# Kernel optimization log

Hardware: AMD Instinct MI355X
Metric: run time of the kernel (lower is better)

## Reference

```python
import jax, jax.numpy as jnp
import numpy as np

B, S, H = 4, 2048, 1024
N_EXPERTS = 8
EXPERT_DIM = 1024  # must equal H (see module: wo features = expert_dim, output added to zeros_like(x))
TOP_K = 2
Z_LOSS_COEF = 0.001


def setup_inputs() -> dict:
    key = jax.random.key(0)
    ks = jax.random.split(key, 8)
    s_h = 1.0 / np.sqrt(H)
    s_e = 1.0 / np.sqrt(EXPERT_DIM)
    return {
        "x": jax.random.normal(ks[0], (B, S, H), dtype=jnp.float32),
        "router_w": jax.random.normal(ks[1], (H, N_EXPERTS), dtype=jnp.float32) * s_h,
        "router_b": jnp.zeros((N_EXPERTS,), dtype=jnp.float32),
        "wi_w": jax.random.normal(ks[2], (N_EXPERTS, H, EXPERT_DIM), dtype=jnp.float32) * s_h,
        "wi_b": jnp.zeros((N_EXPERTS, EXPERT_DIM), dtype=jnp.float32),
        "wo_w": jax.random.normal(ks[3], (N_EXPERTS, EXPERT_DIM, EXPERT_DIM), dtype=jnp.float32) * s_e,
        "wo_b": jnp.zeros((N_EXPERTS, EXPERT_DIM), dtype=jnp.float32),
    }


def reference(x, router_w, router_b, wi_w, wi_b, wo_w, wo_b):
    # Router (deterministic=True: no jitter noise, no dropout)
    logits = jnp.einsum("bsh,he->bse", x, router_w) + router_b        # [B,S,Ne]
    probs = jax.nn.softmax(logits, axis=-1)
    z_loss = jnp.mean(jnp.square(jax.nn.logsumexp(logits, axis=-1))) * Z_LOSS_COEF
    topk_p, topk_i = jax.lax.top_k(probs, TOP_K)                      # [B,S,2]
    topk_p = topk_p / jnp.sum(topk_p, axis=-1, keepdims=True)
    # Faithful to source: mask[...,None] ([B,S,2,1]) broadcasts against x ([B,S,H])
    # producing [B,S,2,H]; combined output has that shape.
    out = jnp.zeros((B, S, TOP_K, H), dtype=x.dtype)
    n_experts = wi_w.shape[0]
    for e in range(n_experts):  # fixed small expert loop, as in source
        mask = (topk_i == e)                                          # [B,S,2]
        p = jnp.where(mask, topk_p, 0.0)                              # [B,S,2]
        xin = jnp.where(mask[..., None], x[:, :, None, :], 0.0)       # [B,S,2,H]
        h = jax.nn.gelu(jnp.einsum("bskh,hd->bskd", xin, wi_w[e]) + wi_b[e])
        y = jnp.einsum("bskd,do->bsko", h, wo_w[e]) + wo_b[e]         # [B,S,2,H]
        out = out + y * p[..., None]
    return out, z_loss
```

## Files before the change

### kernel.cpp

```cpp
#include <hip/hip_runtime.h>

typedef unsigned short u16;
typedef unsigned int   u32;
typedef __bf16 bf16x8 __attribute__((ext_vector_type(8)));
typedef float  f32x4  __attribute__((ext_vector_type(4)));

#define NTOK   8192
#define NSLOT  16384

#define XB_OFF   0UL
#define WIT_OFF  16777216UL
#define WOT_OFF  33554432UL
#define HB_OFF   50331648UL
#define RE_OFF   83886080UL
#define RP_OFF   83951616UL
#define SEG_OFF  84017152UL
#define META_OFF 84082688UL
#define ZB_OFF   (META_OFF + 4096UL)
#define WS_NEED  (ZB_OFF + 32768UL)

__device__ __forceinline__ u16 f2b(float f) {
  u32 u = __float_as_uint(f);
  u32 r = (u + 0x7fffu + ((u >> 16) & 1u)) >> 16;
  return (u16)r;
}

__device__ __forceinline__ void async_cp16(const void* g, void* l) {
  __builtin_amdgcn_global_load_lds(
      (const __attribute__((address_space(1))) u32*)g,
      (__attribute__((address_space(3))) u32*)l, 16, 0, 0);
}

__device__ __forceinline__ float gelu_f(float v) {
  float u  = 0.7978845608028654f * (v + 0.044715f * v * v * v);
  float ex = __expf(2.0f * u);
  float th = 1.0f - 2.0f / (ex + 1.0f);
  return 0.5f * v * (1.0f + th);
}

__global__ __launch_bounds__(256) void k_transpose(const float* __restrict__ wi,
                                                   const float* __restrict__ wo,
                                                   u16* __restrict__ wit,
                                                   u16* __restrict__ wot) {
  __shared__ float t[64][65];
  int z = blockIdx.z;
  int e = z & 7;
  const float* src = ((z < 8) ? wi : wo) + ((size_t)e << 20);
  u16* dst = ((z < 8) ? wit : wot) + ((size_t)e << 20);
  int h0 = blockIdx.y * 64, d0 = blockIdx.x * 64;
  int tid = threadIdx.x;
#pragma unroll
  for (int j = 0; j < 4; j++) {
    int f = tid + 256 * j;
    int r = f >> 4, c4 = f & 15;
    float4 v = *(const float4*)&src[(size_t)(h0 + r) * 1024 + d0 + c4 * 4];
    t[r][c4 * 4 + 0] = v.x; t[r][c4 * 4 + 1] = v.y;
    t[r][c4 * 4 + 2] = v.z; t[r][c4 * 4 + 3] = v.w;
  }
  __syncthreads();
#pragma unroll
  for (int j = 0; j < 4; j++) {
    int f = tid + 256 * j;
    int d = f >> 4, c4 = f & 15;
    u32 p0 = (u32)f2b(t[c4 * 4 + 0][d]) | ((u32)f2b(t[c4 * 4 + 1][d]) << 16);
    u32 p1 = (u32)f2b(t[c4 * 4 + 2][d]) | ((u32)f2b(t[c4 * 4 + 3][d]) << 16);
    u32* dp = (u32*)&dst[(size_t)(d0 + d) * 1024 + h0 + c4 * 4];
    dp[0] = p0; dp[1] = p1;
  }
}

__global__ __launch_bounds__(256) void k_router(const float* __restrict__ x,
    const float* __restrict__ rw, const float* __restrict__ rb,
    u16* __restrict__ xb, int* __restrict__ route_e, float* __restrict__ route_p,
    float* __restrict__ zbuf) {
  int wv = blockIdx.x * 4 + (threadIdx.x >> 6);
  int l = threadIdx.x & 63;
#pragma unroll 1
  for (int t = 0; t < 4; t++) {
    int tok = wv * 4 + t;
    const float* xrow = x + (size_t)tok * 1024;
    u16* xbrow = xb + (size_t)tok * 1024;
    float a[8] = {0.f, 0.f, 0.f, 0.f, 0.f, 0.f, 0.f, 0.f};
#pragma unroll
    for (int j = 0; j < 16; j++) {
      int c = j * 64 + l;
      float xj = xrow[c];
      xbrow[c] = f2b(xj);
      float4 w0 = *(const float4*)&rw[c * 8];
      float4 w1 = *(const float4*)&rw[c * 8 + 4];
      a[0] += xj * w0.x; a[1] += xj * w0.y; a[2] += xj * w0.z; a[3] += xj * w0.w;
      a[4] += xj * w1.x; a[5] += xj * w1.y; a[6] += xj * w1.z; a[7] += xj * w1.w;
    }
#pragma unroll
    for (int e = 0; e < 8; e++)
#pragma unroll
      for (int off = 32; off; off >>= 1) a[e] += __shfl_xor(a[e], off, 64);
    if (l == 0) {
#pragma unroll
      for (int e = 0; e < 8; e++) a[e] += rb[e];
      int e0 = 0; float b0 = a[0];
#pragma unroll
      for (int k = 1; k < 8; k++) if (a[k] > b0) { b0 = a[k]; e0 = k; }
      int e1 = -1; float b1 = -3.4e38f;
#pragma unroll
      for (int k = 0; k < 8; k++) { if (k == e0) continue; if (a[k] > b1) { b1 = a[k]; e1 = k; } }
      float s = 0.f;
#pragma unroll
      for (int k = 0; k < 8; k++) s += __expf(a[k] - b0);
      float lse = b0 + __logf(s);
      float q1 = __expf(b1 - b0);
      route_e[tok * 2 + 0] = e0; route_e[tok * 2 + 1] = e1;
      route_p[tok * 2 + 0] = 1.0f / (1.0f + q1);
      route_p[tok * 2 + 1] = q1 / (1.0f + q1);
      zbuf[tok] = lse * lse;
    }
  }
}

__global__ __launch_bounds__(256) void k_scan(
    const int* __restrict__ route_e, int* __restrict__ offs,
    int* __restrict__ cursors, int* __restrict__ ntiles,
    int* __restrict__ tile_e, int* __restrict__ tile_r0,
    const float* __restrict__ zbuf, float* __restrict__ zout) {
  __shared__ int cnt[8];
  __shared__ float zs[4];
  int tid = threadIdx.x;
  if (tid < 8) cnt[tid] = 0;
  __syncthreads();
  for (int i = tid; i < NSLOT; i += 256) atomicAdd(&cnt[route_e[i]], 1);
  float z = 0.f;
  for (int i = tid; i < NTOK; i += 256) z += zbuf[i];
#pragma unroll
  for (int off = 32; off; off >>= 1) z += __shfl_xor(z, off, 64);
  if ((tid & 63) == 0) zs[tid >> 6] = z;
  __syncthreads();
  if (tid == 0) {
    *zout = (zs[0] + zs[1] + zs[2] + zs[3]) * (0.001f / 8192.0f);
    int o = 0, nt = 0;
    offs[0] = 0;
    for (int e = 0; e < 8; e++) {
      int c = cnt[e];
      cursors[e] = o;
      for (int r = 0; r < c; r += 320) { tile_e[nt] = e; tile_r0[nt] = o + r; nt++; }
      o += c;
      offs[e + 1] = o;
    }
    *ntiles = nt;
  }
}

__global__ __launch_bounds__(256) void k_scatter(const int* __restrict__ route_e,
                                                 int* __restrict__ cursors,
                                                 int* __restrict__ seg) {
  int i = blockIdx.x * 256 + threadIdx.x;
  int e = route_e[i];
  int lane = threadIdx.x & 63;
#pragma unroll
  for (int ex = 0; ex < 8; ex++) {
    unsigned long long mask = __ballot(e == ex);
    if (e == ex) {
      int cnt = __popcll(mask);
      int leader = __ffsll((long long)mask) - 1;
      int base = 0;
      if (lane == leader) base = atomicAdd(&cursors[ex], cnt);
      base = __shfl(base, leader, 64);
      int rank = __popcll(mask & ((1ull << lane) - 1ull));
      seg[base + rank] = i;
    }
  }
}


#define BAR()    asm volatile("s_barrier" ::: "memory")
#define WAITV0() asm volatile("s_waitcnt vmcnt(0)" ::: "memory")

#define STAGE_A(B, KT, J) async_cp16(asrc[J] + (KT) * 64, &As[B][(w * 40 + (J) * 8) * 64])
#define STAGE_B(B, KT, J) async_cp16(bsrc[J] + (KT) * 64, &Bs[B][(w * 32 + (J) * 8) * 64])

#define PHASE(CUR, Q)                                                              \
  do {                                                                             \
    bf16x8 af[2][2], bfr[2][4];                                                    \
    _Pragma("unroll")                                                              \
    for (int kk = 0; kk < 2; kk++) {                                               \
      int c = ((kk * 4 + rh) ^ (rl & 7)) * 8;                                      \
      _Pragma("unroll")                                                            \
      for (int d = 0; d < 2; d++)                                                  \
        af[kk][d] = *(const bf16x8*)&As[CUR][(wr * 160 + (2 * (Q) + d) * 16 + rl) * 64 + c]; \
      _Pragma("unroll")                                                            \
      for (int n = 0; n < 4; n++)                                                  \
        bfr[kk][n] = *(const bf16x8*)&Bs[CUR][(wc * 64 + n * 16 + rl) * 64 + c];   \
    }                                                                              \
    __builtin_amdgcn_s_setprio(1);                                                 \
    _Pragma("unroll")                                                              \
    for (int kk = 0; kk < 2; kk++)                                                 \
      _Pragma("unroll")                                                            \
      for (int d = 0; d < 2; d++)                                                  \
        _Pragma("unroll")                                                          \
        for (int n = 0; n < 4; n++)                                                \
          acc[2 * (Q) + d][n] = __builtin_amdgcn_mfma_f32_16x16x32_bf16(           \
              af[kk][d], bfr[kk][n], acc[2 * (Q) + d][n], 0, 0, 0);                \
    __builtin_amdgcn_s_setprio(0);                                                 \
  } while (0)

#define GEMM_BODY()                                                                \
  _Pragma("unroll")                                                                \
  for (int j = 0; j < 5; j++) STAGE_A(0, 0, j);                                    \
  _Pragma("unroll")                                                                \
  for (int j = 0; j < 4; j++) STAGE_B(0, 0, j);                                    \
  WAITV0(); BAR();                                                                 \
  _Pragma("unroll 2")                                                              \
  for (int g = 0; g < 16; g++) {                                                   \
    int cur = g & 1, nxt = cur ^ 1;                                                \
    bool pf = (g < 15);                                                            \
    if (pf) { STAGE_A(nxt, g + 1, 0); STAGE_A(nxt, g + 1, 1); STAGE_A(nxt, g + 1, 2); \
              STAGE_B(nxt, g + 1, 0); STAGE_B(nxt, g + 1, 1); }                    \
    PHASE(cur, 0); BAR();                                                          \
    if (pf) { STAGE_A(nxt, g + 1, 3); STAGE_A(nxt, g + 1, 4);                      \
              STAGE_B(nxt, g + 1, 2); STAGE_B(nxt, g + 1, 3); }                    \
    PHASE(cur, 1); BAR();                                                          \
    PHASE(cur, 2); BAR();                                                          \
    PHASE(cur, 3); BAR();                                                          \
    PHASE(cur, 4);                                                                 \
    WAITV0(); BAR();                                                               \
  }

__global__ __launch_bounds__(512, 2) void k_gemm_h(
    const u16* __restrict__ xb, const u16* __restrict__ wit, const float* __restrict__ wib,
    u16* __restrict__ hb, const int* __restrict__ seg, const int* __restrict__ offs,
    const int* __restrict__ tile_e, const int* __restrict__ tile_r0,
    const int* __restrict__ ntiles) {
  __shared__ u16 As[2][320 * 64];
  __shared__ u16 Bs[2][256 * 64];
  int bid = blockIdx.x;
  int swz = (bid & 7) * 30 + (bid >> 3);
  int mt = swz >> 2;
  if (mt >= *ntiles) return;
  int n0 = (swz & 3) << 8;
  int e = tile_e[mt], r0 = tile_r0[mt], end = offs[e + 1];
  int tid = threadIdx.x;
  int w = tid >> 6, l = tid & 63;
  int lr = l >> 3, lc = l & 7;
  int cs = lc ^ lr;
  const u16* asrc[5];
  const u16* bsrc[4];
#pragma unroll
  for (int j = 0; j < 5; j++) {
    int gr = r0 + w * 40 + j * 8 + lr;
    int idx = seg[(gr < end) ? gr : r0];
    asrc[j] = xb + (size_t)(idx >> 1) * 1024 + cs * 8;
  }
#pragma unroll
  for (int j = 0; j < 4; j++)
    bsrc[j] = wit + ((size_t)e << 20) + (size_t)(n0 + w * 32 + j * 8 + lr) * 1024 + cs * 8;
  f32x4 acc[10][4];
  f32x4 z4 = {0.f, 0.f, 0.f, 0.f};
#pragma unroll
  for (int m = 0; m < 10; m++)
#pragma unroll
    for (int n = 0; n < 4; n++) acc[m][n] = z4;
  int wr = w >> 2, wc = w & 3;
  int rl = l & 15, rh = l >> 4;
  GEMM_BODY()
#pragma unroll
  for (int n = 0; n < 4; n++) {
    int col = n0 + wc * 64 + n * 16 + rl;
    float bias = wib[e * 1024 + col];
#pragma unroll
    for (int m = 0; m < 10; m++) {
      int rbase = r0 + wr * 160 + m * 16 + rh * 4;
#pragma unroll
      for (int j = 0; j < 4; j++) {
        int gr = rbase + j;
        if (gr < end)
          hb[(size_t)gr * 1024 + col] = f2b(gelu_f(acc[m][n][j] + bias));
      }
    }
  }
}

__global__ __launch_bounds__(512, 2) void k_gemm_o(
    const u16* __restrict__ hb, const u16* __restrict__ wot, const float* __restrict__ wob,
    float* __restrict__ out, const int* __restrict__ seg, const int* __restrict__ offs,
    const int* __restrict__ tile_e, const int* __restrict__ tile_r0,
    const int* __restrict__ ntiles, const float* __restrict__ route_p) {
  __shared__ u16 As[2][320 * 64];
  __shared__ u16 Bs[2][256 * 64];
  int bid = blockIdx.x;
  int swz = (bid & 7) * 30 + (bid >> 3);
  int mt = swz >> 2;
  if (mt >= *ntiles) return;
  int n0 = (swz & 3) << 8;
  int e = tile_e[mt], r0 = tile_r0[mt], end = offs[e + 1];
  int tid = threadIdx.x;
  int w = tid >> 6, l = tid & 63;
  int lr = l >> 3, lc = l & 7;
  int cs = lc ^ lr;
  const u16* asrc[5];
  const u16* bsrc[4];
#pragma unroll
  for (int j = 0; j < 5; j++) {
    int gr = r0 + w * 40 + j * 8 + lr;
    int grc = (gr < end) ? gr : r0;
    asrc[j] = hb + (size_t)grc * 1024 + cs * 8;
  }
#pragma unroll
  for (int j = 0; j < 4; j++)
    bsrc[j] = wot + ((size_t)e << 20) + (size_t)(n0 + w * 32 + j * 8 + lr) * 1024 + cs * 8;
  f32x4 acc[10][4];
  f32x4 z4 = {0.f, 0.f, 0.f, 0.f};
#pragma unroll
  for (int m = 0; m < 10; m++)
#pragma unroll
    for (int n = 0; n < 4; n++) acc[m][n] = z4;
  int wr = w >> 2, wc = w & 3;
  int rl = l & 15, rh = l >> 4;
  GEMM_BODY()
#pragma unroll
  for (int m = 0; m < 10; m++) {
    int rbase = r0 + wr * 160 + m * 16 + rh * 4;
#pragma unroll
    for (int j = 0; j < 4; j++) {
      int gr = rbase + j;
      if (gr >= end) continue;
      int idx = seg[gr];
      float p = route_p[idx];
      float* orow = out + (size_t)idx * 1024;
#pragma unroll
      for (int n = 0; n < 4; n++) {
        int col = n0 + wc * 64 + n * 16 + rl;
        orow[col] = (acc[m][n][j] + wob[e * 1024 + col]) * p;
      }
    }
  }
}

extern "C" void kernel_launch(void* const* d_in, const int* in_sizes, int n_in,
                              void* d_out, int out_size, void* d_ws, size_t ws_size,
                              hipStream_t stream) {
  if (ws_size < WS_NEED) return;
  const float* x   = (const float*)d_in[0];
  const float* rw  = (const float*)d_in[1];
  const float* rb  = (const float*)d_in[2];
  const float* wiw = (const float*)d_in[3];
  const float* wib = (const float*)d_in[4];
  const float* wow = (const float*)d_in[5];
  const float* wob = (const float*)d_in[6];
  float* out = (float*)d_out;
  char* ws = (char*)d_ws;

  u16*   xb      = (u16*)(ws + XB_OFF);
  u16*   wit     = (u16*)(ws + WIT_OFF);
  u16*   wot     = (u16*)(ws + WOT_OFF);
  u16*   hb      = (u16*)(ws + HB_OFF);
  int*   route_e = (int*)(ws + RE_OFF);
  float* route_p = (float*)(ws + RP_OFF);
  int*   seg     = (int*)(ws + SEG_OFF);
  int*   offs    = (int*)(ws + META_OFF + 64);
  int*   cursors = (int*)(ws + META_OFF + 128);
  int*   ntiles  = (int*)(ws + META_OFF + 192);
  int*   tile_e  = (int*)(ws + META_OFF + 256);
  int*   tile_r0 = (int*)(ws + META_OFF + 1024);
  float* zbuf    = (float*)(ws + ZB_OFF);

  k_transpose<<<dim3(16, 16, 16), 256, 0, stream>>>(wiw, wow, wit, wot);
  k_router<<<512, 256, 0, stream>>>(x, rw, rb, xb, route_e, route_p, zbuf);
  k_scan<<<1, 256, 0, stream>>>(route_e, offs, cursors, ntiles, tile_e, tile_r0,
                                zbuf, out + (out_size - 1));
  k_scatter<<<64, 256, 0, stream>>>(route_e, cursors, seg);
  k_gemm_h<<<240, 512, 0, stream>>>(xb, wit, wib, hb, seg, offs,
                                    tile_e, tile_r0, ntiles);
  k_gemm_o<<<240, 512, 0, stream>>>(hb, wot, wob, out, seg, offs,
                                    tile_e, tile_r0, ntiles, route_p);
}
```

Baseline: 223.6 us.

## Shrink expert GEMM M-tile to 128 rows and simplify to single-buffered loop

Reduces the expert GEMM row tile from 320 to 128 slots, raising the grid from 240 to 544 blocks and the accumulator count from 10x4 to 4x4 per wave. The double-buffered, phase-interleaved prefetch pipeline with priority hints is replaced by a simple load, sync, compute, sync loop on a single LDS buffer. The aim is more parallelism, better load balance across experts and less padding waste. The cost is no overlap of global loads with MFMA work and lower arithmetic intensity per tile, since weight tiles are reloaded more often.

```diff
diff --git a/kernel.cpp b/kernel.cpp
--- a/kernel.cpp
+++ b/kernel.cpp
@@ -141,7 +141,7 @@
     for (int e = 0; e < 8; e++) {
       int c = cnt[e];
       cursors[e] = o;
-      for (int r = 0; r < c; r += 320) { tile_e[nt] = e; tile_r0[nt] = o + r; nt++; }
+      for (int r = 0; r < c; r += 128) { tile_e[nt] = e; tile_r0[nt] = o + r; nt++; }
       o += c;
       offs[e + 1] = o;
     }
@@ -171,68 +171,50 @@
 }
 
 
-#define BAR()    asm volatile("s_barrier" ::: "memory")
-#define WAITV0() asm volatile("s_waitcnt vmcnt(0)" ::: "memory")
-
-#define STAGE_A(B, KT, J) async_cp16(asrc[J] + (KT) * 64, &As[B][(w * 40 + (J) * 8) * 64])
-#define STAGE_B(B, KT, J) async_cp16(bsrc[J] + (KT) * 64, &Bs[B][(w * 32 + (J) * 8) * 64])
-
-#define PHASE(CUR, Q)                                                              \
-  do {                                                                             \
-    bf16x8 af[2][2], bfr[2][4];                                                    \
+#define STAGE_ALL(KT)                                                    \
+  do {                                                                   \
+    async_cp16(asrc[0] + (KT) * 64, &As[(w * 16 + 0) * 64]);             \
+    async_cp16(asrc[1] + (KT) * 64, &As[(w * 16 + 8) * 64]);             \
+    async_cp16(bsrc[0] + (KT) * 64, &Bs[(w * 32 + 0) * 64]);             \
+    async_cp16(bsrc[1] + (KT) * 64, &Bs[(w * 32 + 8) * 64]);             \
+    async_cp16(bsrc[2] + (KT) * 64, &Bs[(w * 32 + 16) * 64]);            \
+    async_cp16(bsrc[3] + (KT) * 64, &Bs[(w * 32 + 24) * 64]);            \
+  } while (0)
+
+#define GEMM_BODY()                                                                \
+  _Pragma("unroll 1")                                                              \
+  for (int kt = 0; kt < 16; kt++) {                                                \
+    STAGE_ALL(kt);                                                                 \
+    __syncthreads();                                                               \
     _Pragma("unroll")                                                              \
     for (int kk = 0; kk < 2; kk++) {                                               \
       int c = ((kk * 4 + rh) ^ (rl & 7)) * 8;                                      \
+      bf16x8 af[4], bfr[4];                                                        \
       _Pragma("unroll")                                                            \
-      for (int d = 0; d < 2; d++)                                                  \
-        af[kk][d] = *(const bf16x8*)&As[CUR][(wr * 160 + (2 * (Q) + d) * 16 + rl) * 64 + c]; \
+      for (int m = 0; m < 4; m++)                                                  \
+        af[m] = *(const bf16x8*)&As[(wr * 64 + m * 16 + rl) * 64 + c];             \
       _Pragma("unroll")                                                            \
       for (int n = 0; n < 4; n++)                                                  \
-        bfr[kk][n] = *(const bf16x8*)&Bs[CUR][(wc * 64 + n * 16 + rl) * 64 + c];   \
-    }                                                                              \
-    __builtin_amdgcn_s_setprio(1);                                                 \
-    _Pragma("unroll")                                                              \
-    for (int kk = 0; kk < 2; kk++)                                                 \
+        bfr[n] = *(const bf16x8*)&Bs[(wc * 64 + n * 16 + rl) * 64 + c];            \
       _Pragma("unroll")                                                            \
-      for (int d = 0; d < 2; d++)                                                  \
+      for (int m = 0; m < 4; m++)                                                  \
         _Pragma("unroll")                                                          \
         for (int n = 0; n < 4; n++)                                                \
-          acc[2 * (Q) + d][n] = __builtin_amdgcn_mfma_f32_16x16x32_bf16(           \
-              af[kk][d], bfr[kk][n], acc[2 * (Q) + d][n], 0, 0, 0);                \
-    __builtin_amdgcn_s_setprio(0);                                                 \
-  } while (0)
-
-#define GEMM_BODY()                                                                \
-  _Pragma("unroll")                                                                \
-  for (int j = 0; j < 5; j++) STAGE_A(0, 0, j);                                    \
-  _Pragma("unroll")                                                                \
-  for (int j = 0; j < 4; j++) STAGE_B(0, 0, j);                                    \
-  WAITV0(); BAR();                                                                 \
-  _Pragma("unroll 2")                                                              \
-  for (int g = 0; g < 16; g++) {                                                   \
-    int cur = g & 1, nxt = cur ^ 1;                                                \
-    bool pf = (g < 15);                                                            \
-    if (pf) { STAGE_A(nxt, g + 1, 0); STAGE_A(nxt, g + 1, 1); STAGE_A(nxt, g + 1, 2); \
-              STAGE_B(nxt, g + 1, 0); STAGE_B(nxt, g + 1, 1); }                    \
-    PHASE(cur, 0); BAR();                                                          \
-    if (pf) { STAGE_A(nxt, g + 1, 3); STAGE_A(nxt, g + 1, 4);                      \
-              STAGE_B(nxt, g + 1, 2); STAGE_B(nxt, g + 1, 3); }                    \
-    PHASE(cur, 1); BAR();                                                          \
-    PHASE(cur, 2); BAR();                                                          \
-    PHASE(cur, 3); BAR();                                                          \
-    PHASE(cur, 4);                                                                 \
-    WAITV0(); BAR();                                                               \
-  }
-
-__global__ __launch_bounds__(512, 2) void k_gemm_h(
+          acc[m][n] = __builtin_amdgcn_mfma_f32_16x16x32_bf16(af[m], bfr[n],       \
+                                                              acc[m][n], 0, 0, 0); \
+    }                                                                              \
+    __syncthreads();                                                               \
+  }
+
+__global__ __launch_bounds__(512) void k_gemm_h(
     const u16* __restrict__ xb, const u16* __restrict__ wit, const float* __restrict__ wib,
     u16* __restrict__ hb, const int* __restrict__ seg, const int* __restrict__ offs,
     const int* __restrict__ tile_e, const int* __restrict__ tile_r0,
     const int* __restrict__ ntiles) {
-  __shared__ u16 As[2][320 * 64];
-  __shared__ u16 Bs[2][256 * 64];
+  __shared__ u16 As[128 * 64];
+  __shared__ u16 Bs[256 * 64];
   int bid = blockIdx.x;
-  int swz = (bid & 7) * 30 + (bid >> 3);
+  int swz = (bid & 7) * 68 + (bid >> 3);
   int mt = swz >> 2;
   if (mt >= *ntiles) return;
   int n0 = (swz & 3) << 8;
@@ -241,21 +223,21 @@
   int w = tid >> 6, l = tid & 63;
   int lr = l >> 3, lc = l & 7;
   int cs = lc ^ lr;
-  const u16* asrc[5];
+  const u16* asrc[2];
   const u16* bsrc[4];
 #pragma unroll
-  for (int j = 0; j < 5; j++) {
-    int gr = r0 + w * 40 + j * 8 + lr;
+  for (int j = 0; j < 2; j++) {
+    int gr = r0 + w * 16 + j * 8 + lr;
     int idx = seg[(gr < end) ? gr : r0];
     asrc[j] = xb + (size_t)(idx >> 1) * 1024 + cs * 8;
   }
 #pragma unroll
   for (int j = 0; j < 4; j++)
     bsrc[j] = wit + ((size_t)e << 20) + (size_t)(n0 + w * 32 + j * 8 + lr) * 1024 + cs * 8;
-  f32x4 acc[10][4];
+  f32x4 acc[4][4];
   f32x4 z4 = {0.f, 0.f, 0.f, 0.f};
 #pragma unroll
-  for (int m = 0; m < 10; m++)
+  for (int m = 0; m < 4; m++)
 #pragma unroll
     for (int n = 0; n < 4; n++) acc[m][n] = z4;
   int wr = w >> 2, wc = w & 3;
@@ -266,8 +248,8 @@
     int col = n0 + wc * 64 + n * 16 + rl;
     float bias = wib[e * 1024 + col];
 #pragma unroll
-    for (int m = 0; m < 10; m++) {
-      int rbase = r0 + wr * 160 + m * 16 + rh * 4;
+    for (int m = 0; m < 4; m++) {
+      int rbase = r0 + wr * 64 + m * 16 + rh * 4;
 #pragma unroll
       for (int j = 0; j < 4; j++) {
         int gr = rbase + j;
@@ -278,15 +260,15 @@
   }
 }
 
-__global__ __launch_bounds__(512, 2) void k_gemm_o(
+__global__ __launch_bounds__(512) void k_gemm_o(
     const u16* __restrict__ hb, const u16* __restrict__ wot, const float* __restrict__ wob,
     float* __restrict__ out, const int* __restrict__ seg, const int* __restrict__ offs,
     const int* __restrict__ tile_e, const int* __restrict__ tile_r0,
     const int* __restrict__ ntiles, const float* __restrict__ route_p) {
-  __shared__ u16 As[2][320 * 64];
-  __shared__ u16 Bs[2][256 * 64];
+  __shared__ u16 As[128 * 64];
+  __shared__ u16 Bs[256 * 64];
   int bid = blockIdx.x;
-  int swz = (bid & 7) * 30 + (bid >> 3);
+  int swz = (bid & 7) * 68 + (bid >> 3);
   int mt = swz >> 2;
   if (mt >= *ntiles) return;
   int n0 = (swz & 3) << 8;
@@ -295,29 +277,29 @@
   int w = tid >> 6, l = tid & 63;
   int lr = l >> 3, lc = l & 7;
   int cs = lc ^ lr;
-  const u16* asrc[5];
+  const u16* asrc[2];
   const u16* bsrc[4];
 #pragma unroll
-  for (int j = 0; j < 5; j++) {
-    int gr = r0 + w * 40 + j * 8 + lr;
+  for (int j = 0; j < 2; j++) {
+    int gr = r0 + w * 16 + j * 8 + lr;
     int grc = (gr < end) ? gr : r0;
     asrc[j] = hb + (size_t)grc * 1024 + cs * 8;
   }
 #pragma unroll
   for (int j = 0; j < 4; j++)
     bsrc[j] = wot + ((size_t)e << 20) + (size_t)(n0 + w * 32 + j * 8 + lr) * 1024 + cs * 8;
-  f32x4 acc[10][4];
+  f32x4 acc[4][4];
   f32x4 z4 = {0.f, 0.f, 0.f, 0.f};
 #pragma unroll
-  for (int m = 0; m < 10; m++)
+  for (int m = 0; m < 4; m++)
 #pragma unroll
     for (int n = 0; n < 4; n++) acc[m][n] = z4;
   int wr = w >> 2, wc = w & 3;
   int rl = l & 15, rh = l >> 4;
   GEMM_BODY()
 #pragma unroll
-  for (int m = 0; m < 10; m++) {
-    int rbase = r0 + wr * 160 + m * 16 + rh * 4;
+  for (int m = 0; m < 4; m++) {
+    int rbase = r0 + wr * 64 + m * 16 + rh * 4;
 #pragma unroll
     for (int j = 0; j < 4; j++) {
       int gr = rbase + j;
@@ -367,8 +349,8 @@
   k_scan<<<1, 256, 0, stream>>>(route_e, offs, cursors, ntiles, tile_e, tile_r0,
                                 zbuf, out + (out_size - 1));
   k_scatter<<<64, 256, 0, stream>>>(route_e, cursors, seg);
-  k_gemm_h<<<240, 512, 0, stream>>>(xb, wit, wib, hb, seg, offs,
+  k_gemm_h<<<544, 512, 0, stream>>>(xb, wit, wib, hb, seg, offs,
                                     tile_e, tile_r0, ntiles);
-  k_gemm_o<<<240, 512, 0, stream>>>(hb, wot, wob, out, seg, offs,
+  k_gemm_o<<<544, 512, 0, stream>>>(hb, wot, wob, out, seg, offs,
                                     tile_e, tile_r0, ntiles, route_p);
 }
```

Result: no change. 220.5 us (-1.4%).

## Restructure expert GEMM pipeline with triple-buffered B ring and register-staged A

Applied to the files above, without the earlier changes.

Replaces the double-buffered async LDS staging of both operands with a three-deep LDS ring for the weight (B) tiles and register-staged loads for the gathered activation (A) tiles, which go into a single LDS buffer. Prefetch runs two K-steps ahead, with partial vmcnt waits instead of full drains, and barriers per K-tile drop from five to two. The MFMA loop is reordered so each A fragment feeds four B fragments per region. This aims to hide global latency better and cut barrier stalls, at the cost of more registers (ten uint4 A staging registers), which could hurt occupancy under launch_bounds(512,2). It also depends on the vmcnt wait counts matching the number of loads in flight exactly.

```diff
diff --git a/kernel.cpp b/kernel.cpp
--- a/kernel.cpp
+++ b/kernel.cpp
@@ -171,57 +171,99 @@
 }
 
 
-#define BAR()    asm volatile("s_barrier" ::: "memory")
-#define WAITV0() asm volatile("s_waitcnt vmcnt(0)" ::: "memory")
-
-#define STAGE_A(B, KT, J) async_cp16(asrc[J] + (KT) * 64, &As[B][(w * 40 + (J) * 8) * 64])
-#define STAGE_B(B, KT, J) async_cp16(bsrc[J] + (KT) * 64, &Bs[B][(w * 32 + (J) * 8) * 64])
-
-#define PHASE(CUR, Q)                                                              \
-  do {                                                                             \
-    bf16x8 af[2][2], bfr[2][4];                                                    \
-    _Pragma("unroll")                                                              \
-    for (int kk = 0; kk < 2; kk++) {                                               \
-      int c = ((kk * 4 + rh) ^ (rl & 7)) * 8;                                      \
-      _Pragma("unroll")                                                            \
-      for (int d = 0; d < 2; d++)                                                  \
-        af[kk][d] = *(const bf16x8*)&As[CUR][(wr * 160 + (2 * (Q) + d) * 16 + rl) * 64 + c]; \
-      _Pragma("unroll")                                                            \
-      for (int n = 0; n < 4; n++)                                                  \
-        bfr[kk][n] = *(const bf16x8*)&Bs[CUR][(wc * 64 + n * 16 + rl) * 64 + c];   \
-    }                                                                              \
-    __builtin_amdgcn_s_setprio(1);                                                 \
-    _Pragma("unroll")                                                              \
-    for (int kk = 0; kk < 2; kk++)                                                 \
-      _Pragma("unroll")                                                            \
-      for (int d = 0; d < 2; d++)                                                  \
-        _Pragma("unroll")                                                          \
-        for (int n = 0; n < 4; n++)                                                \
-          acc[2 * (Q) + d][n] = __builtin_amdgcn_mfma_f32_16x16x32_bf16(           \
-              af[kk][d], bfr[kk][n], acc[2 * (Q) + d][n], 0, 0, 0);                \
-    __builtin_amdgcn_s_setprio(0);                                                 \
+#define BTILE (256 * 64)
+
+#define W9()  asm volatile("s_waitcnt vmcnt(9)" ::: "memory")
+#define W5()  asm volatile("s_waitcnt vmcnt(5)" ::: "memory")
+#define W0()  asm volatile("s_waitcnt vmcnt(0)" ::: "memory")
+#define LG0() asm volatile("s_waitcnt lgkmcnt(0)" ::: "memory")
+#define BAR() asm volatile("s_barrier" ::: "memory")
+
+#define STAGE_B_RING(BSW, KT)                                     \
+  do {                                                            \
+    async_cp16(bsrc[0] + (KT) * 64, (BSW) + (w * 32 +  0) * 64);  \
+    async_cp16(bsrc[1] + (KT) * 64, (BSW) + (w * 32 +  8) * 64);  \
+    async_cp16(bsrc[2] + (KT) * 64, (BSW) + (w * 32 + 16) * 64);  \
+    async_cp16(bsrc[3] + (KT) * 64, (BSW) + (w * 32 + 24) * 64);  \
   } while (0)
 
-#define GEMM_BODY()                                                                \
-  _Pragma("unroll")                                                                \
-  for (int j = 0; j < 5; j++) STAGE_A(0, 0, j);                                    \
-  _Pragma("unroll")                                                                \
-  for (int j = 0; j < 4; j++) STAGE_B(0, 0, j);                                    \
-  WAITV0(); BAR();                                                                 \
-  _Pragma("unroll 2")                                                              \
-  for (int g = 0; g < 16; g++) {                                                   \
-    int cur = g & 1, nxt = cur ^ 1;                                                \
-    bool pf = (g < 15);                                                            \
-    if (pf) { STAGE_A(nxt, g + 1, 0); STAGE_A(nxt, g + 1, 1); STAGE_A(nxt, g + 1, 2); \
-              STAGE_B(nxt, g + 1, 0); STAGE_B(nxt, g + 1, 1); }                    \
-    PHASE(cur, 0); BAR();                                                          \
-    if (pf) { STAGE_A(nxt, g + 1, 3); STAGE_A(nxt, g + 1, 4);                      \
-              STAGE_B(nxt, g + 1, 2); STAGE_B(nxt, g + 1, 3); }                    \
-    PHASE(cur, 1); BAR();                                                          \
-    PHASE(cur, 2); BAR();                                                          \
-    PHASE(cur, 3); BAR();                                                          \
-    PHASE(cur, 4);                                                                 \
-    WAITV0(); BAR();                                                               \
+#define LOAD_A_REGS(AR, KT)                                       \
+  do {                                                            \
+    _Pragma("unroll")                                             \
+    for (int j = 0; j < 5; j++)                                   \
+      AR[j] = *(const uint4*)(const void*)(asrc[j] + (KT) * 64);  \
+  } while (0)
+
+#define WRITE_A_LDS(AR)                                                    \
+  do {                                                                     \
+    _Pragma("unroll")                                                      \
+    for (int j = 0; j < 5; j++)                                            \
+      *(uint4*)(void*)&As[(w * 40 + j * 8 + lr) * 64 + lc * 8] = AR[j];    \
+  } while (0)
+
+#define REGION(BSR, KK, MH)                                                \
+  do {                                                                     \
+    int c = (((KK) * 4 + rh) ^ (rl & 7)) * 8;                              \
+    if ((MH) == 0) {                                                       \
+      _Pragma("unroll")                                                    \
+      for (int n = 0; n < 4; n++)                                          \
+        bfr[(KK)][n] = *(const bf16x8*)&(BSR)[(wc * 64 + n * 16 + rl) * 64 + c]; \
+    }                                                                      \
+    bf16x8 af[5];                                                          \
+    _Pragma("unroll")                                                      \
+    for (int m = 0; m < 5; m++)                                            \
+      af[m] = *(const bf16x8*)&As[(wr * 160 + ((MH) * 5 + m) * 16 + rl) * 64 + c]; \
+    __builtin_amdgcn_s_setprio(1);                                         \
+    _Pragma("unroll")                                                      \
+    for (int m = 0; m < 5; m++)                                            \
+      _Pragma("unroll")                                                    \
+      for (int n = 0; n < 4; n++)                                          \
+        acc[(MH) * 5 + m][n] = __builtin_amdgcn_mfma_f32_16x16x32_bf16(    \
+            af[m], bfr[(KK)][n], acc[(MH) * 5 + m][n], 0, 0, 0);           \
+    __builtin_amdgcn_s_setprio(0);                                         \
+  } while (0)
+
+#define TILE(KT, ARL, ARW, PF, WAITM)                                      \
+  do {                                                                     \
+    const u16* BsR = Bs0 + srd;                                            \
+    if (PF) {                                                              \
+      u16* bsw = Bs0 + swd;                                                \
+      STAGE_B_RING(bsw, (KT) + 2);                                         \
+      LOAD_A_REGS(ARL, (KT) + 2);                                          \
+    }                                                                      \
+    REGION(BsR, 0, 0); REGION(BsR, 0, 1);                                  \
+    REGION(BsR, 1, 0); REGION(BsR, 1, 1);                                  \
+    WAITM();                                                               \
+    BAR();                                                                 \
+    WRITE_A_LDS(ARW);                                                      \
+    LG0();                                                                 \
+    BAR();                                                                 \
+    srd = (srd == 2 * BTILE) ? 0 : srd + BTILE;                            \
+    swd = (swd == 2 * BTILE) ? 0 : swd + BTILE;                            \
+  } while (0)
+
+#define GEMM_BODY()                                                        \
+  uint4 ar0[5], ar1[5];                                                    \
+  bf16x8 bfr[2][4];                                                        \
+  int srd = 0, swd = 2 * BTILE;                                            \
+  STAGE_B_RING(Bs0, 0);                                                    \
+  STAGE_B_RING(Bs0 + BTILE, 1);                                            \
+  LOAD_A_REGS(ar0, 0);                                                     \
+  LOAD_A_REGS(ar1, 1);                                                     \
+  W5();                           \
+  WRITE_A_LDS(ar0);                                                        \
+  LG0();                                                                   \
+  BAR();                                                                   \
+  _Pragma("unroll 1")                                                      \
+  for (int t = 0; t < 14; t += 2) {                                        \
+    TILE(t,     ar0, ar1, 1, W9);                                          \
+    TILE(t + 1, ar1, ar0, 1, W9);                                          \
+  }                                                                        \
+  TILE(14, ar0, ar1, 0, W0);                                               \
+  {                                                                        \
+    const u16* BsR = Bs0 + srd;                                            \
+    REGION(BsR, 0, 0); REGION(BsR, 0, 1);                                  \
+    REGION(BsR, 1, 0); REGION(BsR, 1, 1);                                  \
   }
 
 __global__ __launch_bounds__(512, 2) void k_gemm_h(
@@ -229,8 +271,9 @@
     u16* __restrict__ hb, const int* __restrict__ seg, const int* __restrict__ offs,
     const int* __restrict__ tile_e, const int* __restrict__ tile_r0,
     const int* __restrict__ ntiles) {
-  __shared__ u16 As[2][320 * 64];
-  __shared__ u16 Bs[2][256 * 64];
+  __shared__ u16 As[320 * 64];
+  __shared__ u16 Bs[3][256 * 64];
+  u16* Bs0 = &Bs[0][0];
   int bid = blockIdx.x;
   int swz = (bid & 7) * 30 + (bid >> 3);
   int mt = swz >> 2;
@@ -283,8 +326,9 @@
     float* __restrict__ out, const int* __restrict__ seg, const int* __restrict__ offs,
     const int* __restrict__ tile_e, const int* __restrict__ tile_r0,
     const int* __restrict__ ntiles, const float* __restrict__ route_p) {
-  __shared__ u16 As[2][320 * 64];
-  __shared__ u16 Bs[2][256 * 64];
+  __shared__ u16 As[320 * 64];
+  __shared__ u16 Bs[3][256 * 64];
+  u16* Bs0 = &Bs[0][0];
   int bid = blockIdx.x;
   int swz = (bid & 7) * 30 + (bid >> 3);
   int mt = swz >> 2;
```

Result: slower. 254.6 us (+13.9%).

## Merge weight transpose and router kernels; hoist B fragment loads per k-step

Applied to the files above, without the earlier changes.

Combines the weight transpose/bf16 conversion and the router into one launch, with a block-index split, so the two independent prep stages run concurrently and one launch is saved. In the GEMM body, the B-tile fragments are loaded from LDS once per k-step and reused across all five A phases instead of being reloaded in every phase. This cuts LDS read traffic in the GEMMs, but it keeps 8 more bf16x8 registers live across the phases, which may raise register pressure at 2 blocks per CU.

```diff
diff --git a/kernel.cpp b/kernel.cpp
--- a/kernel.cpp
+++ b/kernel.cpp
@@ -38,81 +38,80 @@
   return 0.5f * v * (1.0f + th);
 }
 
-__global__ __launch_bounds__(256) void k_transpose(const float* __restrict__ wi,
-                                                   const float* __restrict__ wo,
-                                                   u16* __restrict__ wit,
-                                                   u16* __restrict__ wot) {
-  __shared__ float t[64][65];
-  int z = blockIdx.z;
-  int e = z & 7;
-  const float* src = ((z < 8) ? wi : wo) + ((size_t)e << 20);
-  u16* dst = ((z < 8) ? wit : wot) + ((size_t)e << 20);
-  int h0 = blockIdx.y * 64, d0 = blockIdx.x * 64;
+__global__ __launch_bounds__(256) void k_prep(const float* __restrict__ wi,
+    const float* __restrict__ wo, u16* __restrict__ wit, u16* __restrict__ wot,
+    const float* __restrict__ x, const float* __restrict__ rw,
+    const float* __restrict__ rb, u16* __restrict__ xb,
+    int* __restrict__ route_e, float* __restrict__ route_p,
+    float* __restrict__ zbuf) {
+  int bid = blockIdx.x;
   int tid = threadIdx.x;
-#pragma unroll
-  for (int j = 0; j < 4; j++) {
-    int f = tid + 256 * j;
-    int r = f >> 4, c4 = f & 15;
-    float4 v = *(const float4*)&src[(size_t)(h0 + r) * 1024 + d0 + c4 * 4];
-    t[r][c4 * 4 + 0] = v.x; t[r][c4 * 4 + 1] = v.y;
-    t[r][c4 * 4 + 2] = v.z; t[r][c4 * 4 + 3] = v.w;
-  }
-  __syncthreads();
-#pragma unroll
-  for (int j = 0; j < 4; j++) {
-    int f = tid + 256 * j;
-    int d = f >> 4, c4 = f & 15;
-    u32 p0 = (u32)f2b(t[c4 * 4 + 0][d]) | ((u32)f2b(t[c4 * 4 + 1][d]) << 16);
-    u32 p1 = (u32)f2b(t[c4 * 4 + 2][d]) | ((u32)f2b(t[c4 * 4 + 3][d]) << 16);
-    u32* dp = (u32*)&dst[(size_t)(d0 + d) * 1024 + h0 + c4 * 4];
-    dp[0] = p0; dp[1] = p1;
-  }
-}
-
-__global__ __launch_bounds__(256) void k_router(const float* __restrict__ x,
-    const float* __restrict__ rw, const float* __restrict__ rb,
-    u16* __restrict__ xb, int* __restrict__ route_e, float* __restrict__ route_p,
-    float* __restrict__ zbuf) {
-  int wv = blockIdx.x * 4 + (threadIdx.x >> 6);
-  int l = threadIdx.x & 63;
+  if (bid < 4096) {
+    __shared__ float t[64][65];
+    int e = (bid >> 8) & 7;
+    const float* src = ((bid < 2048) ? wi : wo) + ((size_t)e << 20);
+    u16* dst = ((bid < 2048) ? wit : wot) + ((size_t)e << 20);
+    int h0 = ((bid >> 4) & 15) * 64, d0 = (bid & 15) * 64;
+#pragma unroll
+    for (int j = 0; j < 4; j++) {
+      int f = tid + 256 * j;
+      int r = f >> 4, c4 = f & 15;
+      float4 v = *(const float4*)&src[(size_t)(h0 + r) * 1024 + d0 + c4 * 4];
+      t[r][c4 * 4 + 0] = v.x; t[r][c4 * 4 + 1] = v.y;
+      t[r][c4 * 4 + 2] = v.z; t[r][c4 * 4 + 3] = v.w;
+    }
+    __syncthreads();
+#pragma unroll
+    for (int j = 0; j < 4; j++) {
+      int f = tid + 256 * j;
+      int d = f >> 4, c4 = f & 15;
+      u32 p0 = (u32)f2b(t[c4 * 4 + 0][d]) | ((u32)f2b(t[c4 * 4 + 1][d]) << 16);
+      u32 p1 = (u32)f2b(t[c4 * 4 + 2][d]) | ((u32)f2b(t[c4 * 4 + 3][d]) << 16);
+      u32* dp = (u32*)&dst[(size_t)(d0 + d) * 1024 + h0 + c4 * 4];
+      dp[0] = p0; dp[1] = p1;
+    }
+  } else {
+    int wv = (bid - 4096) * 4 + (tid >> 6);
+    int l = tid & 63;
 #pragma unroll 1
-  for (int t = 0; t < 4; t++) {
-    int tok = wv * 4 + t;
-    const float* xrow = x + (size_t)tok * 1024;
-    u16* xbrow = xb + (size_t)tok * 1024;
-    float a[8] = {0.f, 0.f, 0.f, 0.f, 0.f, 0.f, 0.f, 0.f};
-#pragma unroll
-    for (int j = 0; j < 16; j++) {
-      int c = j * 64 + l;
-      float xj = xrow[c];
-      xbrow[c] = f2b(xj);
-      float4 w0 = *(const float4*)&rw[c * 8];
-      float4 w1 = *(const float4*)&rw[c * 8 + 4];
-      a[0] += xj * w0.x; a[1] += xj * w0.y; a[2] += xj * w0.z; a[3] += xj * w0.w;
-      a[4] += xj * w1.x; a[5] += xj * w1.y; a[6] += xj * w1.z; a[7] += xj * w1.w;
-    }
-#pragma unroll
-    for (int e = 0; e < 8; e++)
-#pragma unroll
-      for (int off = 32; off; off >>= 1) a[e] += __shfl_xor(a[e], off, 64);
-    if (l == 0) {
-#pragma unroll
-      for (int e = 0; e < 8; e++) a[e] += rb[e];
-      int e0 = 0; float b0 = a[0];
-#pragma unroll
-      for (int k = 1; k < 8; k++) if (a[k] > b0) { b0 = a[k]; e0 = k; }
-      int e1 = -1; float b1 = -3.4e38f;
-#pragma unroll
-      for (int k = 0; k < 8; k++) { if (k == e0) continue; if (a[k] > b1) { b1 = a[k]; e1 = k; } }
-      float s = 0.f;
-#pragma unroll
-      for (int k = 0; k < 8; k++) s += __expf(a[k] - b0);
-      float lse = b0 + __logf(s);
-      float q1 = __expf(b1 - b0);
-      route_e[tok * 2 + 0] = e0; route_e[tok * 2 + 1] = e1;
-      route_p[tok * 2 + 0] = 1.0f / (1.0f + q1);
-      route_p[tok * 2 + 1] = q1 / (1.0f + q1);
-      zbuf[tok] = lse * lse;
+    for (int t4 = 0; t4 < 4; t4++) {
+      int tok = wv * 4 + t4;
+      const float* xrow = x + (size_t)tok * 1024;
+      u16* xbrow = xb + (size_t)tok * 1024;
+      float a[8] = {0.f, 0.f, 0.f, 0.f, 0.f, 0.f, 0.f, 0.f};
+#pragma unroll
+      for (int j = 0; j < 16; j++) {
+        int c = j * 64 + l;
+        float xj = xrow[c];
+        xbrow[c] = f2b(xj);
+        float4 w0 = *(const float4*)&rw[c * 8];
+        float4 w1 = *(const float4*)&rw[c * 8 + 4];
+        a[0] += xj * w0.x; a[1] += xj * w0.y; a[2] += xj * w0.z; a[3] += xj * w0.w;
+        a[4] += xj * w1.x; a[5] += xj * w1.y; a[6] += xj * w1.z; a[7] += xj * w1.w;
+      }
+#pragma unroll
+      for (int e = 0; e < 8; e++)
+#pragma unroll
+        for (int off = 32; off; off >>= 1) a[e] += __shfl_xor(a[e], off, 64);
+      if (l == 0) {
+#pragma unroll
+        for (int e = 0; e < 8; e++) a[e] += rb[e];
+        int e0 = 0; float b0 = a[0];
+#pragma unroll
+        for (int k = 1; k < 8; k++) if (a[k] > b0) { b0 = a[k]; e0 = k; }
+        int e1 = -1; float b1 = -3.4e38f;
+#pragma unroll
+        for (int k = 0; k < 8; k++) { if (k == e0) continue; if (a[k] > b1) { b1 = a[k]; e1 = k; } }
+        float s = 0.f;
+#pragma unroll
+        for (int k = 0; k < 8; k++) s += __expf(a[k] - b0);
+        float lse = b0 + __logf(s);
+        float q1 = __expf(b1 - b0);
+        route_e[tok * 2 + 0] = e0; route_e[tok * 2 + 1] = e1;
+        route_p[tok * 2 + 0] = 1.0f / (1.0f + q1);
+        route_p[tok * 2 + 1] = q1 / (1.0f + q1);
+        zbuf[tok] = lse * lse;
+      }
     }
   }
 }
@@ -177,18 +176,26 @@
 #define STAGE_A(B, KT, J) async_cp16(asrc[J] + (KT) * 64, &As[B][(w * 40 + (J) * 8) * 64])
 #define STAGE_B(B, KT, J) async_cp16(bsrc[J] + (KT) * 64, &Bs[B][(w * 32 + (J) * 8) * 64])
 
+#define PHASE_BLOAD(CUR)                                                           \
+  do {                                                                             \
+    _Pragma("unroll")                                                              \
+    for (int kk = 0; kk < 2; kk++) {                                               \
+      int c = ((kk * 4 + rh) ^ (rl & 7)) * 8;                                      \
+      _Pragma("unroll")                                                            \
+      for (int n = 0; n < 4; n++)                                                  \
+        bfr[kk][n] = *(const bf16x8*)&Bs[CUR][(wc * 64 + n * 16 + rl) * 64 + c];   \
+    }                                                                              \
+  } while (0)
+
 #define PHASE(CUR, Q)                                                              \
   do {                                                                             \
-    bf16x8 af[2][2], bfr[2][4];                                                    \
+    bf16x8 af[2][2];                                                               \
     _Pragma("unroll")                                                              \
     for (int kk = 0; kk < 2; kk++) {                                               \
       int c = ((kk * 4 + rh) ^ (rl & 7)) * 8;                                      \
       _Pragma("unroll")                                                            \
       for (int d = 0; d < 2; d++)                                                  \
         af[kk][d] = *(const bf16x8*)&As[CUR][(wr * 160 + (2 * (Q) + d) * 16 + rl) * 64 + c]; \
-      _Pragma("unroll")                                                            \
-      for (int n = 0; n < 4; n++)                                                  \
-        bfr[kk][n] = *(const bf16x8*)&Bs[CUR][(wc * 64 + n * 16 + rl) * 64 + c];   \
     }                                                                              \
     __builtin_amdgcn_s_setprio(1);                                                 \
     _Pragma("unroll")                                                              \
@@ -212,8 +219,10 @@
   for (int g = 0; g < 16; g++) {                                                   \
     int cur = g & 1, nxt = cur ^ 1;                                                \
     bool pf = (g < 15);                                                            \
+    bf16x8 bfr[2][4];                                                              \
     if (pf) { STAGE_A(nxt, g + 1, 0); STAGE_A(nxt, g + 1, 1); STAGE_A(nxt, g + 1, 2); \
               STAGE_B(nxt, g + 1, 0); STAGE_B(nxt, g + 1, 1); }                    \
+    PHASE_BLOAD(cur);                                                              \
     PHASE(cur, 0); BAR();                                                          \
     if (pf) { STAGE_A(nxt, g + 1, 3); STAGE_A(nxt, g + 1, 4);                      \
               STAGE_B(nxt, g + 1, 2); STAGE_B(nxt, g + 1, 3); }                    \
@@ -362,8 +371,8 @@
   int*   tile_r0 = (int*)(ws + META_OFF + 1024);
   float* zbuf    = (float*)(ws + ZB_OFF);
 
-  k_transpose<<<dim3(16, 16, 16), 256, 0, stream>>>(wiw, wow, wit, wot);
-  k_router<<<512, 256, 0, stream>>>(x, rw, rb, xb, route_e, route_p, zbuf);
+  k_prep<<<4608, 256, 0, stream>>>(wiw, wow, wit, wot, x, rw, rb, xb,
+                                   route_e, route_p, zbuf);
   k_scan<<<1, 256, 0, stream>>>(route_e, offs, cursors, ntiles, tile_e, tile_r0,
                                 zbuf, out + (out_size - 1));
   k_scatter<<<64, 256, 0, stream>>>(route_e, cursors, seg);
```

New measurement: 224.7 us. About the same (+0.5%).
